# Performance work log

Hardware: AMD Instinct MI355X
Metric: run time of the kernel (lower is better)

The kernel has to match this reference:

```python
import jax, jax.numpy as jnp
import numpy as np

NEG = -1e9  # max-semiring 'zero' / structural mask value


def _cky_max(pot, lengths):
    """Max-plus CKY inside pass (torch_struct CKY_CRF with MaxSemiring).

    pot: [B, N, N] label-maxed span potentials, pot[b, i, j] = score of span (i, j).
    Returns [B] best binary-tree score for each sequence of given length.
    betaA[b, i, w]      = best score of span starting at i with width w (span [i, i+w]).
    betaB[b, j, N-1-w]  = best score of span ending at j with width w.
    """
    B, N, _ = pot.shape
    term = jnp.diagonal(pot, axis1=1, axis2=2)  # [B, N] width-0 spans
    betaA = jnp.full((B, N, N), NEG, dtype=pot.dtype).at[:, :, 0].set(term)
    betaB = jnp.full((B, N, N), NEG, dtype=pot.dtype).at[:, :, N - 1].set(term)
    for w in range(1, N):
        Y = betaA[:, : N - w, :w]       # [B, N-w, w] left children, widths 0..w-1
        Z = betaB[:, w:, N - w:]        # [B, N-w, w] right children (matching splits)
        span = jnp.diagonal(pot, offset=w, axis1=1, axis2=2)  # [B, N-w] pot[b, i, i+w]
        new = jnp.max(Y + Z, axis=-1) + span
        betaA = betaA.at[:, : N - w, w].set(new)
        betaB = betaB.at[:, w:, N - w - 1].set(new)
    final = betaA[:, 0, :]  # [B, N]: final[b, l-1] = best tree over [0, l-1]
    return final[jnp.arange(B), lengths - 1]


def setup_inputs() -> dict:
    key = jax.random.key(0)
    k1, k2 = jax.random.split(key)
    B, N, L = 64, 128, 32
    logits = jax.random.normal(k1, (B, N, N, L), dtype=jnp.float32)
    labels = jax.random.randint(k2, (B, N, N), 0, L, dtype=jnp.int64)
    return {"logits": logits, "labels": labels}


def reference(logits, labels):
    B, N, _, L = logits.shape
    gold_event = jax.nn.one_hot(jnp.maximum(labels, 0), L, dtype=logits.dtype)
    logits = logits - logits[..., :1]
    lengths = jnp.sum(labels[:, 0, :] != -100, axis=-1)
    augment = 1.0 - gold_event
    # force_root_constituent=True: forbid non-constituent root span
    augment = augment.at[jnp.arange(B), 0, lengths - 1, 0].add(-1e9)
    pot = jnp.max(logits + augment, axis=-1)  # max-semiring sum over label dim
    pred_score = _cky_max(pot, lengths)                      # [B]
    gold_score = jnp.sum(logits * gold_event, axis=(1, 2, 3))  # [B]
    margin_losses = jax.nn.relu(pred_score - gold_score)
    return jnp.mean(margin_losses)
```

## Files before the change

### kernel.cpp

```cpp
#include <hip/hip_runtime.h>

#define BATCH 64
#define SEQ   128
#define NLAB  32
#define NEGF  -3.0e38f

__global__ __launch_bounds__(64) void len_kernel(
    const int* __restrict__ labels, int* __restrict__ lenbuf)
{
    const int b = blockIdx.x;
    const int t = threadIdx.x;
    const size_t base = (size_t)b * SEQ * SEQ;
    int cnt = (labels[base + t] != -100) + (labels[base + 64 + t] != -100);
    #pragma unroll
    for (int d = 32; d; d >>= 1) cnt += __shfl_down(cnt, d, 64);
    if (t == 0) lenbuf[b] = cnt;
}

__global__ __launch_bounds__(256) void pot_gold_kernel(
    const float* __restrict__ logits, const int* __restrict__ labels,
    const int* __restrict__ lenbuf,
    float* __restrict__ pot, float* __restrict__ gold)
{
    const int c = blockIdx.x * 256 + threadIdx.x;
    const int b = c >> 14;
    const int ij = c & (SEQ * SEQ - 1);
    const int i = ij >> 7;
    const int j = ij & (SEQ - 1);

    const float4* src = reinterpret_cast<const float4*>(logits) + ((size_t)c << 3);
    float4 f[8];
    #pragma unroll
    for (int t = 0; t < 8; ++t) f[t] = src[t];

    const int lab_raw = labels[c];
    const int lab = lab_raw < 0 ? 0 : lab_raw;
    const int len = lenbuf[b];
    const bool special = (i == 0) && (j == len - 1);

    const float l0 = f[0].x;
    float m = NEGF, g = 0.0f;
    #pragma unroll
    for (int t = 0; t < 8; ++t) {
        const float vv[4] = { f[t].x, f[t].y, f[t].z, f[t].w };
        #pragma unroll
        for (int cc = 0; cc < 4; ++cc) {
            const int l = t * 4 + cc;
            const float r = vv[cc] - l0;
            const bool isg = (l == lab);
            g = isg ? r : g;
            float cand = r + (isg ? 0.0f : 1.0f);
            if (special && l == 0) cand -= 1.0e9f;
            m = fmaxf(m, cand);
        }
    }
    pot[c] = m;

    #pragma unroll
    for (int d = 32; d; d >>= 1) g += __shfl_down(g, d, 64);
    __shared__ float s_red[4];
    if ((threadIdx.x & 63) == 0) s_red[threadIdx.x >> 6] = g;
    __syncthreads();
    if (threadIdx.x == 0)
        atomicAdd(&gold[b], s_red[0] + s_red[1] + s_red[2] + s_red[3]);
}

__global__ __launch_bounds__(512, 1) void cky_kernel(
    const float* __restrict__ pot, const float* __restrict__ gold,
    const int* __restrict__ lenbuf, float* __restrict__ out)
{
    const int b = blockIdx.x;
    const int tid = threadIdx.x;
    const float* p = pot + (size_t)b * SEQ * SEQ;

    constexpr int PITCH = 132;
    __shared__ __align__(16) float S[2 * SEQ * PITCH];
    float* Abase = S;
    float* Bbase = S + SEQ * PITCH;

    {
        const float4 neg4 = make_float4(NEGF, NEGF, NEGF, NEGF);
        float4* s4 = reinterpret_cast<float4*>(S);
        for (int idx = tid; idx < 2 * SEQ * PITCH / 4; idx += 512) s4[idx] = neg4;
    }
    __syncthreads();
    if (tid < SEQ) {
        const float term = p[tid * (SEQ + 1)];
        Abase[tid * PITCH] = term;
        Bbase[tid * PITCH] = term;
    }
    __syncthreads();

    float potv;
    {
        int e1 = SEQ - 1;
        int i1 = tid >> 2;
        if (i1 >= e1) i1 = e1 - 1;
        potv = p[i1 * (SEQ + 1) + 1];
    }

    for (int w = 1; w < SEQ; ++w) {
        const int entries = SEQ - w;
        int tpe = 1, lt = 0;
        while (tpe < 64 && ((tpe << 1) * entries) <= 512) { tpe <<= 1; ++lt; }
        const int i = tid >> lt;
        const int s = tid & (tpe - 1);

        float pot_next = 0.0f;
        if (w + 1 < SEQ) {
            const int e2 = SEQ - (w + 1);
            int tpe2 = 1, lt2 = 0;
            while (tpe2 < 64 && ((tpe2 << 1) * e2) <= 512) { tpe2 <<= 1; ++lt2; }
            int i2 = tid >> lt2;
            if (i2 >= e2) i2 = e2 - 1;
            pot_next = p[i2 * (SEQ + 1) + (w + 1)];
        }

        if (i < entries) {
            float* Arow = Abase + i * PITCH;
            float* Brow = Bbase + (i + w) * PITCH;
            const int wq = (w + 3) >> 2;
            float m = NEGF;
            int q = s;
            for (; q + tpe < wq; q += 2 * tpe) {
                const int k0 = q << 2, k1 = (q + tpe) << 2;
                float4 a0 = *reinterpret_cast<const float4*>(Arow + k0);
                float4 a1 = *reinterpret_cast<const float4*>(Arow + k1);
                const float b00 = Brow[w - 1 - k0], b01 = Brow[w - 2 - k0],
                            b02 = Brow[w - 3 - k0], b03 = Brow[w - 4 - k0];
                const float b10 = Brow[w - 1 - k1], b11 = Brow[w - 2 - k1],
                            b12 = Brow[w - 3 - k1], b13 = Brow[w - 4 - k1];
                if (k1 + 4 > w) {
                    a1.y = (k1 + 1 < w) ? a1.y : NEGF;
                    a1.z = (k1 + 2 < w) ? a1.z : NEGF;
                    a1.w = (k1 + 3 < w) ? a1.w : NEGF;
                }
                m = fmaxf(m, fmaxf(fmaxf(a0.x + b00, a0.y + b01),
                                   fmaxf(a0.z + b02, a0.w + b03)));
                m = fmaxf(m, fmaxf(fmaxf(a1.x + b10, a1.y + b11),
                                   fmaxf(a1.z + b12, a1.w + b13)));
            }
            if (q < wq) {
                const int k0 = q << 2;
                float4 a0 = *reinterpret_cast<const float4*>(Arow + k0);
                const float b00 = Brow[w - 1 - k0], b01 = Brow[w - 2 - k0],
                            b02 = Brow[w - 3 - k0], b03 = Brow[w - 4 - k0];
                if (k0 + 4 > w) {
                    a0.y = (k0 + 1 < w) ? a0.y : NEGF;
                    a0.z = (k0 + 2 < w) ? a0.z : NEGF;
                    a0.w = (k0 + 3 < w) ? a0.w : NEGF;
                }
                m = fmaxf(m, fmaxf(fmaxf(a0.x + b00, a0.y + b01),
                                   fmaxf(a0.z + b02, a0.w + b03)));
            }
            for (int d = tpe >> 1; d; d >>= 1)
                m = fmaxf(m, __shfl_down(m, d, tpe));
            if (s == 0) {
                const float val = m + potv;
                Arow[w] = val;
                Brow[w] = val;
            }
        }
        potv = pot_next;
        __syncthreads();
    }

    if (tid == 0) {
        const int len = lenbuf[b];
        const float pred = Abase[len - 1];
        float margin = pred - gold[b];
        margin = margin > 0.0f ? margin : 0.0f;
        atomicAdd(out, margin * (1.0f / (float)BATCH));
    }
}

extern "C" void kernel_launch(void* const* d_in, const int* in_sizes, int n_in,
                              void* d_out, int out_size, void* d_ws, size_t ws_size,
                              hipStream_t stream) {
    const float* logits = (const float*)d_in[0];
    const int* labels = (const int*)d_in[1];
    float* out = (float*)d_out;

    float* pot = (float*)d_ws;
    float* gold = pot + (size_t)BATCH * SEQ * SEQ;
    int* lenbuf = (int*)(gold + BATCH);

    (void)hipMemsetAsync(out, 0, sizeof(float), stream);
    (void)hipMemsetAsync(gold, 0, BATCH * sizeof(float), stream);

    len_kernel<<<BATCH, 64, 0, stream>>>(labels, lenbuf);
    pot_gold_kernel<<<BATCH * SEQ * SEQ / 256, 256, 0, stream>>>(
        logits, labels, lenbuf, pot, gold);
    cky_kernel<<<BATCH, 512, 0, stream>>>(pot, gold, lenbuf, out);
}
```

Baseline: 306.8 us.

## Coalesce logits loads via LDS staging and preload span potentials into CKY tables

```diff
diff --git a/kernel.cpp b/kernel.cpp
--- a/kernel.cpp
+++ b/kernel.cpp
@@ -22,47 +22,75 @@
     const int* __restrict__ lenbuf,
     float* __restrict__ pot, float* __restrict__ gold)
 {
-    const int c = blockIdx.x * 256 + threadIdx.x;
-    const int b = c >> 14;
-    const int ij = c & (SEQ * SEQ - 1);
-    const int i = ij >> 7;
-    const int j = ij & (SEQ - 1);
-
-    const float4* src = reinterpret_cast<const float4*>(logits) + ((size_t)c << 3);
-    float4 f[8];
+    const int tid = threadIdx.x;
+    const int wave = tid >> 6, lane = tid & 63;
+    __shared__ __align__(16) float LP[4 * 16 * 36];
+    float* W = LP + wave * (16 * 36);
+
+    const int block_cell0 = blockIdx.x * 256;
+    const int b = block_cell0 >> 14;
+    const int len = lenbuf[b];
+    float gacc = 0.0f;
+
+    const int wave_cell0 = block_cell0 + wave * 64;
+
     #pragma unroll
-    for (int t = 0; t < 8; ++t) f[t] = src[t];
-
-    const int lab_raw = labels[c];
-    const int lab = lab_raw < 0 ? 0 : lab_raw;
-    const int len = lenbuf[b];
-    const bool special = (i == 0) && (j == len - 1);
-
-    const float l0 = f[0].x;
-    float m = NEGF, g = 0.0f;
-    #pragma unroll
-    for (int t = 0; t < 8; ++t) {
-        const float vv[4] = { f[t].x, f[t].y, f[t].z, f[t].w };
+    for (int chunk = 0; chunk < 4; ++chunk) {
+        const int c0 = wave_cell0 + chunk * 16;
+        const float4* src = reinterpret_cast<const float4*>(logits) + ((size_t)c0 << 3);
+        const float4 f0 = src[lane];
+        const float4 f1 = src[lane + 64];
+        const int lv = (lane < 16) ? labels[c0 + lane] : 0;
+
+        {
+            const int cA = lane >> 3, tA = lane & 7;
+            *reinterpret_cast<float4*>(W + cA * 36 + tA * 4) = f0;
+            const int q1 = lane + 64;
+            const int cB = q1 >> 3, tB = q1 & 7;
+            *reinterpret_cast<float4*>(W + cB * 36 + tB * 4) = f1;
+        }
+        const int c = lane >> 2, u = lane & 3;
+        const float4 r0 = *reinterpret_cast<const float4*>(W + c * 36 + u * 8);
+        const float4 r1 = *reinterpret_cast<const float4*>(W + c * 36 + u * 8 + 4);
+
+        int lab = __shfl(lv, c, 64);
+        if (lab < 0) lab = 0;
+        const float l0 = __shfl(r0.x, c << 2, 64);
+
+        const int cell = c0 + c;
+        const int ci = (cell >> 7) & (SEQ - 1);
+        const int cj = cell & (SEQ - 1);
+        const bool special = (ci == 0) && (cj == len - 1);
+
+        const float vv[8] = { r0.x, r0.y, r0.z, r0.w, r1.x, r1.y, r1.z, r1.w };
+        float m = NEGF, g = 0.0f;
         #pragma unroll
-        for (int cc = 0; cc < 4; ++cc) {
-            const int l = t * 4 + cc;
-            const float r = vv[cc] - l0;
+        for (int e = 0; e < 8; ++e) {
+            const int l = u * 8 + e;
+            const float r = vv[e] - l0;
             const bool isg = (l == lab);
             g = isg ? r : g;
             float cand = r + (isg ? 0.0f : 1.0f);
-            if (special && l == 0) cand -= 1.0e9f;
+            if (l == 0 && special) cand -= 1.0e9f;
             m = fmaxf(m, cand);
         }
-    }
-    pot[c] = m;
+        m = fmaxf(m, __shfl_xor(m, 1, 64));
+        m = fmaxf(m, __shfl_xor(m, 2, 64));
+        g += __shfl_xor(g, 1, 64);
+        g += __shfl_xor(g, 2, 64);
+        if (u == 0) {
+            pot[cell] = m;
+            gacc += g;
+        }
+    }
 
     #pragma unroll
-    for (int d = 32; d; d >>= 1) g += __shfl_down(g, d, 64);
-    __shared__ float s_red[4];
-    if ((threadIdx.x & 63) == 0) s_red[threadIdx.x >> 6] = g;
+    for (int d = 1; d < 64; d <<= 1) gacc += __shfl_xor(gacc, d, 64);
+    __shared__ float gred[4];
+    if (lane == 0) gred[wave] = gacc;
     __syncthreads();
-    if (threadIdx.x == 0)
-        atomicAdd(&gold[b], s_red[0] + s_red[1] + s_red[2] + s_red[3]);
+    if (tid == 0)
+        atomicAdd(&gold[b], gred[0] + gred[1] + gred[2] + gred[3]);
 }
 
 __global__ __launch_bounds__(512, 1) void cky_kernel(
@@ -73,31 +101,33 @@
     const int tid = threadIdx.x;
     const float* p = pot + (size_t)b * SEQ * SEQ;
 
-    constexpr int PITCH = 132;
-    __shared__ __align__(16) float S[2 * SEQ * PITCH];
-    float* Abase = S;
-    float* Bbase = S + SEQ * PITCH;
+    __shared__ __align__(16) float A[SEQ * 132];
+    __shared__ __align__(16) float Bt[SEQ * 129];
 
     {
         const float4 neg4 = make_float4(NEGF, NEGF, NEGF, NEGF);
-        float4* s4 = reinterpret_cast<float4*>(S);
-        for (int idx = tid; idx < 2 * SEQ * PITCH / 4; idx += 512) s4[idx] = neg4;
+        float4* a4 = reinterpret_cast<float4*>(A);
+        for (int idx = tid; idx < SEQ * 132 / 4; idx += 512) a4[idx] = neg4;
     }
     __syncthreads();
-    if (tid < SEQ) {
-        const float term = p[tid * (SEQ + 1)];
-        Abase[tid * PITCH] = term;
-        Bbase[tid * PITCH] = term;
+    {
+        const float4* p4 = reinterpret_cast<const float4*>(p);
+        for (int qi = tid; qi < SEQ * SEQ / 4; qi += 512) {
+            const int i = qi >> 5;
+            const int j0 = (qi & 31) << 2;
+            const float4 v = p4[qi];
+            const float vv[4] = { v.x, v.y, v.z, v.w };
+            #pragma unroll
+            for (int c2 = 0; c2 < 4; ++c2) {
+                const int j = j0 + c2;
+                if (j >= i) {
+                    A[i * 132 + (j - i)] = vv[c2];
+                    Bt[(j - i) * 129 + j] = vv[c2];
+                }
+            }
+        }
     }
     __syncthreads();
-
-    float potv;
-    {
-        int e1 = SEQ - 1;
-        int i1 = tid >> 2;
-        if (i1 >= e1) i1 = e1 - 1;
-        potv = p[i1 * (SEQ + 1) + 1];
-    }
 
     for (int w = 1; w < SEQ; ++w) {
         const int entries = SEQ - w;
@@ -106,30 +136,26 @@
         const int i = tid >> lt;
         const int s = tid & (tpe - 1);
 
-        float pot_next = 0.0f;
-        if (w + 1 < SEQ) {
-            const int e2 = SEQ - (w + 1);
-            int tpe2 = 1, lt2 = 0;
-            while (tpe2 < 64 && ((tpe2 << 1) * e2) <= 512) { tpe2 <<= 1; ++lt2; }
-            int i2 = tid >> lt2;
-            if (i2 >= e2) i2 = e2 - 1;
-            pot_next = p[i2 * (SEQ + 1) + (w + 1)];
-        }
-
         if (i < entries) {
-            float* Arow = Abase + i * PITCH;
-            float* Brow = Bbase + (i + w) * PITCH;
+            float* Arow = A + i * 132;
+            const int j = i + w;
+            const float potv = Arow[w];
             const int wq = (w + 3) >> 2;
             float m = NEGF;
             int q = s;
             for (; q + tpe < wq; q += 2 * tpe) {
                 const int k0 = q << 2, k1 = (q + tpe) << 2;
-                float4 a0 = *reinterpret_cast<const float4*>(Arow + k0);
+                const float4 a0 = *reinterpret_cast<const float4*>(Arow + k0);
                 float4 a1 = *reinterpret_cast<const float4*>(Arow + k1);
-                const float b00 = Brow[w - 1 - k0], b01 = Brow[w - 2 - k0],
-                            b02 = Brow[w - 3 - k0], b03 = Brow[w - 4 - k0];
-                const float b10 = Brow[w - 1 - k1], b11 = Brow[w - 2 - k1],
-                            b12 = Brow[w - 3 - k1], b13 = Brow[w - 4 - k1];
+                const float b00 = Bt[(w - 1 - k0) * 129 + j];
+                const float b01 = Bt[(w - 2 - k0) * 129 + j];
+                const float b02 = Bt[(w - 3 - k0) * 129 + j];
+                const float b03 = Bt[(w - 4 - k0) * 129 + j];
+                const int r1 = w - 1 - k1;
+                const float b10 = Bt[r1 * 129 + j];
+                const float b11 = Bt[(r1 > 1 ? r1 - 1 : 0) * 129 + j];
+                const float b12 = Bt[(r1 > 2 ? r1 - 2 : 0) * 129 + j];
+                const float b13 = Bt[(r1 > 3 ? r1 - 3 : 0) * 129 + j];
                 if (k1 + 4 > w) {
                     a1.y = (k1 + 1 < w) ? a1.y : NEGF;
                     a1.z = (k1 + 2 < w) ? a1.z : NEGF;
@@ -143,8 +169,11 @@
             if (q < wq) {
                 const int k0 = q << 2;
                 float4 a0 = *reinterpret_cast<const float4*>(Arow + k0);
-                const float b00 = Brow[w - 1 - k0], b01 = Brow[w - 2 - k0],
-                            b02 = Brow[w - 3 - k0], b03 = Brow[w - 4 - k0];
+                const int r0 = w - 1 - k0;
+                const float b00 = Bt[r0 * 129 + j];
+                const float b01 = Bt[(r0 > 1 ? r0 - 1 : 0) * 129 + j];
+                const float b02 = Bt[(r0 > 2 ? r0 - 2 : 0) * 129 + j];
+                const float b03 = Bt[(r0 > 3 ? r0 - 3 : 0) * 129 + j];
                 if (k0 + 4 > w) {
                     a0.y = (k0 + 1 < w) ? a0.y : NEGF;
                     a0.z = (k0 + 2 < w) ? a0.z : NEGF;
@@ -158,16 +187,15 @@
             if (s == 0) {
                 const float val = m + potv;
                 Arow[w] = val;
-                Brow[w] = val;
-            }
-        }
-        potv = pot_next;
+                Bt[w * 129 + j] = val;
+            }
+        }
         __syncthreads();
     }
 
     if (tid == 0) {
         const int len = lenbuf[b];
-        const float pred = Abase[len - 1];
+        const float pred = A[len - 1];
         float margin = pred - gold[b];
         margin = margin > 0.0f ? margin : 0.0f;
         atomicAdd(out, margin * (1.0f / (float)BATCH));
```

Result: no change. 302.0 us (-1.5%).
